# Performance work log

Hardware: AMD Instinct MI355X
Metric: run time of the kernel (lower is better)

## Reference

```python
import jax, jax.numpy as jnp
import numpy as np

N_NODES = 50000
N_USERS = 10000
N_STATE = 1024
N_T1 = 2048
N_T2 = 2048
N_EDGES = 4096


def setup_inputs() -> dict:
    key = jax.random.key(0)
    ks = jax.random.split(key, 10)
    d = N_STATE
    s_u = jax.random.normal(ks[0], (N_USERS, d), jnp.float32)
    x = jax.random.normal(ks[1], (N_NODES, d), jnp.float32)
    # Deterministic graph on which the original torch code is well-defined:
    # POI node 0 has one outgoing edge (edge 0) to tail node 1.
    # Tail node 1 receives edges from heads [0, 2, 3, ..., N_EDGES] in edge order,
    # so list-order in the torch loop aligns with edge-index order.
    heads = np.concatenate([[0], np.arange(2, N_EDGES + 1)]).astype(np.int64)
    tails = np.ones(N_EDGES, dtype=np.int64)
    edge_index = jnp.asarray(np.stack([heads, tails]))
    edge_attr = jax.random.normal(ks[2], (N_EDGES, d), jnp.float32)
    T = jax.random.normal(ks[3], (N_T1, N_T2), jnp.float32)
    u = lambda k, s: jax.random.uniform(k, s, jnp.float32, -1.0, 1.0)
    W_u = u(ks[4], (d, 1))
    W_p = u(ks[5], (d, 1))
    W_T_1 = u(ks[6], (d, N_T1))
    W_T_2 = u(ks[7], (N_T2, 1))
    b_T = u(ks[8], (d, 1))
    W_p_ = u(ks[9], (1, d))
    return dict(s_u=s_u, x=x, edge_attr=edge_attr, T=T, W_u=W_u, W_p=W_p,
                W_T_1=W_T_1, W_T_2=W_T_2, b_T=b_T, W_p_=W_p_,
                edge_index=edge_index, user_index=7, POI_index=0)


def reference(s_u, x, edge_attr, T, W_u, W_p, W_T_1, W_T_2, b_T, W_p_,
              edge_index, user_index, POI_index):
    N, d = x.shape
    heads, tails = edge_index[0], edge_index[1]
    # temporal context vector: sigmoid(W_T_1 @ T @ W_T_2 + b_T), shape (d,)
    t_vec = jax.nn.sigmoid(W_T_1 @ T @ W_T_2 + b_T)[:, 0]
    cur_user = s_u[user_index]   # (d,)
    cur_POI = x[POI_index]       # (d,)
    # user update: u' = sigmoid(u + W_u * (h_P . T'))
    s_u = s_u.at[user_index].set(
        jax.nn.sigmoid(cur_user + W_u[:, 0] * jnp.dot(cur_POI, t_vec)))
    # visited POI update: h' = sigmoid(h + W_p * (u . T'))
    new_POI = jax.nn.sigmoid(cur_POI + W_p[:, 0] * jnp.dot(cur_user, t_vec))
    x = x.at[POI_index].set(new_POI)
    # tail entities of the visited POI: x[tail] = new_POI + edge_attr[e]
    rel_mask = heads == POI_index
    dummy = jnp.zeros((1, d), x.dtype)
    tgt = jnp.where(rel_mask, tails, N)  # route masked-out edges to dummy row
    x = jnp.concatenate([x, dummy], 0).at[tgt].set(new_POI[None, :] + edge_attr)[:N]
    # neighboring POIs: edges whose tail is in the tail set; replicate the original
    # neigh_rel[POI_index] = False / neigh_index.remove(POI_index) pair, which by
    # construction both drop the edge at position POI_index.
    is_tail = jnp.zeros((N + 1,), bool).at[tgt].set(True)[:N]
    neigh_mask = is_tail[tails].at[POI_index].set(False)  # (E,)
    h_emb = x[heads]                        # (E, d), tail-updated embeddings
    scal = (h_emb - edge_attr) @ W_p_[0]    # (E,)  W_p_ . (x[head] - r)
    vals = jax.nn.sigmoid(h_emb + scal[:, None])
    tgt2 = jnp.where(neigh_mask, heads, N)
    x = jnp.concatenate([x, dummy], 0).at[tgt2].set(vals)[:N]
    return (s_u, x)
```

## Files before the change

### kernel.cpp

```cpp
#include <hip/hip_runtime.h>
#include <math.h>
#include <limits.h>

#define D 1024

typedef float f32x4 __attribute__((ext_vector_type(4)));

__device__ __forceinline__ float sigmoidf_(float v) {
    return 1.0f / (1.0f + expf(-v));
}

__device__ __forceinline__ float block_reduce_sum256(float v) {
    #pragma unroll
    for (int off = 32; off; off >>= 1) v += __shfl_down(v, off, 64);
    __shared__ float sm[4];
    int lane = threadIdx.x & 63, w = threadIdx.x >> 6;
    if (lane == 0) sm[w] = v;
    __syncthreads();
    float s = sm[0] + sm[1] + sm[2] + sm[3];
    __syncthreads();
    return s;
}

__global__ void k_pre(const float* __restrict__ T,
                      const float* __restrict__ w,
                      float* __restrict__ tmp,
                      int* __restrict__ flags,
                      int n_flags, int t4 ) {
    const int tid = threadIdx.x;
    int gid = blockIdx.x * 256 + tid;
    int gsz = gridDim.x * 256;
    for (int i = gid; i < n_flags; i += gsz) flags[i] = -1;

    const int row = blockIdx.x;
    const float4* Tr = (const float4*)(T + (size_t)row * (size_t)(t4 * 4));
    const float4* wv = (const float4*)w;
    float acc = 0.f;
    for (int i = tid; i < t4; i += 256) {
        float4 a = Tr[i], c = wv[i];
        acc += a.x * c.x + a.y * c.y + a.z * c.z + a.w * c.w;
    }
    float s = block_reduce_sum256(acc);
    if (tid == 0) tmp[row] = s;
}

__global__ void k_tvec2(const float* __restrict__ W_T_1,
                        const float* __restrict__ tmp,
                        const float* __restrict__ b_T,
                        const float* __restrict__ x,
                        const float* __restrict__ s_u,
                        const int* __restrict__ user_ptr,
                        const int* __restrict__ POI_ptr,
                        const int* __restrict__ edge_index,
                        int* __restrict__ tail_edge,
                        int* __restrict__ neigh_edge,
                        float* __restrict__ pu_P,
                        float* __restrict__ pu_U,
                        int k4 , int E) {
    const int tid = threadIdx.x;
    if (blockIdx.x == gridDim.x - 1) {
        const int POI = POI_ptr[0];
        for (int e = tid; e < E; e += 256)
            if (edge_index[e] == POI)
                atomicMax(&tail_edge[edge_index[E + e]], e);
        __syncthreads();
        for (int e = tid; e < E; e += 256) {
            if (e == POI) continue;
            int te = atomicMax(&tail_edge[edge_index[E + e]], INT_MIN);
            if (te >= 0) atomicMax(&neigh_edge[edge_index[e]], e);
        }
        return;
    }
    const int row = blockIdx.x;
    const float4* Wr = (const float4*)(W_T_1 + (size_t)row * (size_t)(k4 * 4));
    const float4* tv = (const float4*)tmp;
    float acc = 0.f;
    for (int i = tid; i < k4; i += 256) {
        float4 a = Wr[i], c = tv[i];
        acc += a.x * c.x + a.y * c.y + a.z * c.z + a.w * c.w;
    }
    float s = block_reduce_sum256(acc);
    if (tid == 0) {
        float t = sigmoidf_(s + b_T[row]);
        pu_P[row] = x[(size_t)POI_ptr[0] * D + row] * t;
        pu_U[row] = s_u[(size_t)user_ptr[0] * D + row] * t;
    }
}

__global__ void k_mega8(const float* __restrict__ s_u,
                        const float* __restrict__ x,
                        const float* __restrict__ edge_attr,
                        const float* __restrict__ W_u,
                        const float* __restrict__ W_p,
                        const float* __restrict__ Wp_row,
                        const int* __restrict__ user_ptr,
                        const int* __restrict__ POI_ptr,
                        const int* __restrict__ tail_edge,
                        const int* __restrict__ neigh_edge,
                        const float* __restrict__ pu_P,
                        const float* __restrict__ pu_U,
                        float* __restrict__ out,
                        int N_users, int total_rows) {
    const int tid = threadIdx.x;
    const int base = blockIdx.x * 8;
    const int user = user_ptr[0], POI = POI_ptr[0];

    f32x4 v[8];
    #pragma unroll
    for (int k = 0; k < 8; k++) {
        int r = base + k;
        if (r >= total_rows) continue;
        const float* src = (r < N_users) ? s_u + (size_t)r * D
                                         : x + (size_t)(r - N_users) * D;
        v[k] = *((const f32x4*)src + tid);
    }

    int te[8], ne[8];
    bool sp[8];
    #pragma unroll
    for (int k = 0; k < 8; k++) {
        int r = base + k;
        te[k] = -1; ne[k] = -1; sp[k] = false;
        if (r >= total_rows) continue;
        if (r < N_users) {
            sp[k] = (r == user);
        } else {
            int j = r - N_users;
            te[k] = tail_edge[j];
            ne[k] = neigh_edge[j];
            sp[k] = (te[k] >= 0) || (ne[k] >= 0) || (j == POI);
        }
    }

    #pragma unroll
    for (int k = 0; k < 8; k++) {
        int r = base + k;
        if (r >= total_rows) continue;
        f32x4* dst = (f32x4*)(out + (size_t)r * D) + tid;
        if (!sp[k]) {
            __builtin_nontemporal_store(v[k], dst);
            continue;
        }
        if (r < N_users) {
            f32x4 pp = ((const f32x4*)pu_P)[tid];
            float dotP = block_reduce_sum256(pp.x + pp.y + pp.z + pp.w);
            f32x4 wu = ((const f32x4*)W_u)[tid];
            f32x4 o;
            o.x = sigmoidf_(v[k].x + wu.x * dotP);
            o.y = sigmoidf_(v[k].y + wu.y * dotP);
            o.z = sigmoidf_(v[k].z + wu.z * dotP);
            o.w = sigmoidf_(v[k].w + wu.w * dotP);
            __builtin_nontemporal_store(o, dst);
            continue;
        }
        const int j = r - N_users;
        f32x4 uu = ((const f32x4*)pu_U)[tid];
        float dotU = block_reduce_sum256(uu.x + uu.y + uu.z + uu.w);
        f32x4 xp = ((const f32x4*)(x + (size_t)POI * D))[tid];
        f32x4 wp = ((const f32x4*)W_p)[tid];
        f32x4 np;
        np.x = sigmoidf_(xp.x + wp.x * dotU);
        np.y = sigmoidf_(xp.y + wp.y * dotU);
        np.z = sigmoidf_(xp.z + wp.z * dotU);
        np.w = sigmoidf_(xp.w + wp.w * dotU);
        f32x4 hv;
        if (te[k] >= 0) {
            f32x4 b = ((const f32x4*)(edge_attr + (size_t)te[k] * D))[tid];
            hv = np + b;
        } else if (j == POI) {
            hv = np;
        } else {
            hv = v[k];
        }
        if (ne[k] < 0) {
            __builtin_nontemporal_store(hv, dst);
            continue;
        }
        f32x4 ev = ((const f32x4*)(edge_attr + (size_t)ne[k] * D))[tid];
        f32x4 w = ((const f32x4*)Wp_row)[tid];
        f32x4 dd = hv - ev;
        float acc = dd.x * w.x + dd.y * w.y + dd.z * w.z + dd.w * w.w;
        float scal = block_reduce_sum256(acc);
        f32x4 o;
        o.x = sigmoidf_(hv.x + scal);
        o.y = sigmoidf_(hv.y + scal);
        o.z = sigmoidf_(hv.z + scal);
        o.w = sigmoidf_(hv.w + scal);
        __builtin_nontemporal_store(o, dst);
    }
}

extern "C" void kernel_launch(void* const* d_in, const int* in_sizes, int n_in,
                              void* d_out, int out_size, void* d_ws, size_t ws_size,
                              hipStream_t stream) {
    const float* s_u       = (const float*)d_in[0];
    const float* x         = (const float*)d_in[1];
    const float* edge_attr = (const float*)d_in[2];
    const float* T         = (const float*)d_in[3];
    const float* W_u       = (const float*)d_in[4];
    const float* W_p       = (const float*)d_in[5];
    const float* W_T_1     = (const float*)d_in[6];
    const float* W_T_2     = (const float*)d_in[7];
    const float* b_T       = (const float*)d_in[8];
    const float* W_p_      = (const float*)d_in[9];
    const int*   edge_index = (const int*)d_in[10];
    const int*   user_ptr   = (const int*)d_in[11];
    const int*   POI_ptr    = (const int*)d_in[12];

    const int E       = in_sizes[10] / 2;
    const int N_users = in_sizes[0] / D;
    const int N       = in_sizes[1] / D;
    const int N_T2    = in_sizes[7];
    const int N_T1    = in_sizes[6] / D;

    float* ws_f       = (float*)d_ws;
    float* tmp        = ws_f;
    float* pu_P       = ws_f + N_T1;
    float* pu_U       = pu_P + D;
    int*   tail_edge  = (int*)(pu_U + D);
    int*   neigh_edge = tail_edge + N;

    k_pre<<<N_T1, 256, 0, stream>>>(T, W_T_2, tmp, tail_edge, 2 * N, N_T2 / 4);

    k_tvec2<<<D + 1, 256, 0, stream>>>(W_T_1, tmp, b_T, x, s_u, user_ptr,
                                       POI_ptr, edge_index, tail_edge,
                                       neigh_edge, pu_P, pu_U, N_T1 / 4, E);

    const int total_rows = N_users + N;
    k_mega8<<<(total_rows + 7) / 8, 256, 0, stream>>>(
        s_u, x, edge_attr, W_u, W_p, W_p_, user_ptr, POI_ptr,
        tail_edge, neigh_edge, pu_P, pu_U, (float*)d_out, N_users, total_rows);
}
```

Before: 126.5 us.

## Split fused row kernel into bulk streaming copy plus sparse edge-fix kernel

Replaces the per-row mega kernel, which loaded every row and checked per-row flags, with a grid-stride nontemporal copy of s_u and x into the output. A second kernel, launched with one block per edge plus one extra block, then overwrites only the user row, the POI row and the rows touched by edges. The intent is to make the dominant copy a simple bandwidth-bound stream without per-row flag reads or branches. The cost is an extra launch and rows being written twice, and correctness now depends on the fix kernel running after the copy and on the per-edge predicates choosing exactly one writer per row.

```diff
diff --git a/kernel.cpp b/kernel.cpp
--- a/kernel.cpp
+++ b/kernel.cpp
@@ -87,96 +87,98 @@
     }
 }
 
-__global__ void k_mega8(const float* __restrict__ s_u,
-                        const float* __restrict__ x,
-                        const float* __restrict__ edge_attr,
-                        const float* __restrict__ W_u,
-                        const float* __restrict__ W_p,
-                        const float* __restrict__ Wp_row,
-                        const int* __restrict__ user_ptr,
-                        const int* __restrict__ POI_ptr,
-                        const int* __restrict__ tail_edge,
-                        const int* __restrict__ neigh_edge,
-                        const float* __restrict__ pu_P,
-                        const float* __restrict__ pu_U,
-                        float* __restrict__ out,
-                        int N_users, int total_rows) {
+__global__ void k_copy(const f32x4* __restrict__ su,
+                       const f32x4* __restrict__ xx,
+                       f32x4* __restrict__ out,
+                       int n4_su, int n4_x) {
+    const int gid = blockIdx.x * 256 + threadIdx.x;
+    const int gsz = gridDim.x * 256;
+    for (int i = gid; i < n4_su; i += gsz)
+        __builtin_nontemporal_store(__builtin_nontemporal_load(su + i), out + i);
+    f32x4* out_x = out + n4_su;
+    for (int i = gid; i < n4_x; i += gsz)
+        __builtin_nontemporal_store(__builtin_nontemporal_load(xx + i), out_x + i);
+}
+
+__global__ void k_fix(const float* __restrict__ s_u,
+                      const float* __restrict__ x,
+                      const float* __restrict__ edge_attr,
+                      const float* __restrict__ W_u,
+                      const float* __restrict__ W_p,
+                      const float* __restrict__ Wp_row,
+                      const int* __restrict__ user_ptr,
+                      const int* __restrict__ POI_ptr,
+                      const int* __restrict__ edge_index,
+                      const int* __restrict__ tail_edge,
+                      const int* __restrict__ neigh_edge,
+                      const float* __restrict__ pu_P,
+                      const float* __restrict__ pu_U,
+                      float* __restrict__ out,
+                      int N_users, int E) {
+    const int e = blockIdx.x;
     const int tid = threadIdx.x;
-    const int base = blockIdx.x * 8;
-    const int user = user_ptr[0], POI = POI_ptr[0];
-
-    f32x4 v[8];
-    #pragma unroll
-    for (int k = 0; k < 8; k++) {
-        int r = base + k;
-        if (r >= total_rows) continue;
-        const float* src = (r < N_users) ? s_u + (size_t)r * D
-                                         : x + (size_t)(r - N_users) * D;
-        v[k] = *((const f32x4*)src + tid);
-    }
-
-    int te[8], ne[8];
-    bool sp[8];
-    #pragma unroll
-    for (int k = 0; k < 8; k++) {
-        int r = base + k;
-        te[k] = -1; ne[k] = -1; sp[k] = false;
-        if (r >= total_rows) continue;
-        if (r < N_users) {
-            sp[k] = (r == user);
-        } else {
-            int j = r - N_users;
-            te[k] = tail_edge[j];
-            ne[k] = neigh_edge[j];
-            sp[k] = (te[k] >= 0) || (ne[k] >= 0) || (j == POI);
+    const int POI = POI_ptr[0];
+    float* out_x = out + (size_t)N_users * D;
+
+    if (e == E) {
+        const int user = user_ptr[0];
+        f32x4 pp = ((const f32x4*)pu_P)[tid];
+        float dotP = block_reduce_sum256(pp.x + pp.y + pp.z + pp.w);
+        f32x4 uv = ((const f32x4*)(s_u + (size_t)user * D))[tid];
+        f32x4 wu = ((const f32x4*)W_u)[tid];
+        f32x4 o;
+        o.x = sigmoidf_(uv.x + wu.x * dotP);
+        o.y = sigmoidf_(uv.y + wu.y * dotP);
+        o.z = sigmoidf_(uv.z + wu.z * dotP);
+        o.w = sigmoidf_(uv.w + wu.w * dotP);
+        __builtin_nontemporal_store(o, (f32x4*)(out + (size_t)user * D) + tid);
+        if (tail_edge[POI] < 0 && neigh_edge[POI] < 0) {
+            f32x4 uu = ((const f32x4*)pu_U)[tid];
+            float dotU = block_reduce_sum256(uu.x + uu.y + uu.z + uu.w);
+            f32x4 xp = ((const f32x4*)(x + (size_t)POI * D))[tid];
+            f32x4 wp = ((const f32x4*)W_p)[tid];
+            f32x4 np;
+            np.x = sigmoidf_(xp.x + wp.x * dotU);
+            np.y = sigmoidf_(xp.y + wp.y * dotU);
+            np.z = sigmoidf_(xp.z + wp.z * dotU);
+            np.w = sigmoidf_(xp.w + wp.w * dotU);
+            __builtin_nontemporal_store(np, (f32x4*)(out_x + (size_t)POI * D) + tid);
         }
-    }
-
-    #pragma unroll
-    for (int k = 0; k < 8; k++) {
-        int r = base + k;
-        if (r >= total_rows) continue;
-        f32x4* dst = (f32x4*)(out + (size_t)r * D) + tid;
-        if (!sp[k]) {
-            __builtin_nontemporal_store(v[k], dst);
-            continue;
-        }
-        if (r < N_users) {
-            f32x4 pp = ((const f32x4*)pu_P)[tid];
-            float dotP = block_reduce_sum256(pp.x + pp.y + pp.z + pp.w);
-            f32x4 wu = ((const f32x4*)W_u)[tid];
-            f32x4 o;
-            o.x = sigmoidf_(v[k].x + wu.x * dotP);
-            o.y = sigmoidf_(v[k].y + wu.y * dotP);
-            o.z = sigmoidf_(v[k].z + wu.z * dotP);
-            o.w = sigmoidf_(v[k].w + wu.w * dotP);
-            __builtin_nontemporal_store(o, dst);
-            continue;
-        }
-        const int j = r - N_users;
-        f32x4 uu = ((const f32x4*)pu_U)[tid];
-        float dotU = block_reduce_sum256(uu.x + uu.y + uu.z + uu.w);
-        f32x4 xp = ((const f32x4*)(x + (size_t)POI * D))[tid];
-        f32x4 wp = ((const f32x4*)W_p)[tid];
-        f32x4 np;
-        np.x = sigmoidf_(xp.x + wp.x * dotU);
-        np.y = sigmoidf_(xp.y + wp.y * dotU);
-        np.z = sigmoidf_(xp.z + wp.z * dotU);
-        np.w = sigmoidf_(xp.w + wp.w * dotU);
+        return;
+    }
+
+    const int h = edge_index[e], t = edge_index[E + e];
+    const bool tail_w  = (h == POI) && (tail_edge[t] == e) && (neigh_edge[t] < 0);
+    const bool neigh_w = (e != POI) && (tail_edge[t] >= 0) && (neigh_edge[h] == e);
+    if (!tail_w && !neigh_w) return;
+
+    f32x4 uu = ((const f32x4*)pu_U)[tid];
+    float dotU = block_reduce_sum256(uu.x + uu.y + uu.z + uu.w);
+    f32x4 xp = ((const f32x4*)(x + (size_t)POI * D))[tid];
+    f32x4 wp = ((const f32x4*)W_p)[tid];
+    f32x4 np;
+    np.x = sigmoidf_(xp.x + wp.x * dotU);
+    np.y = sigmoidf_(xp.y + wp.y * dotU);
+    np.z = sigmoidf_(xp.z + wp.z * dotU);
+    np.w = sigmoidf_(xp.w + wp.w * dotU);
+
+    if (tail_w) {
+        f32x4 b = ((const f32x4*)(edge_attr + (size_t)e * D))[tid];
+        __builtin_nontemporal_store(np + b, (f32x4*)(out_x + (size_t)t * D) + tid);
+    }
+
+    if (neigh_w) {
         f32x4 hv;
-        if (te[k] >= 0) {
-            f32x4 b = ((const f32x4*)(edge_attr + (size_t)te[k] * D))[tid];
+        const int be = tail_edge[h];
+        if (be >= 0) {
+            f32x4 b = ((const f32x4*)(edge_attr + (size_t)be * D))[tid];
             hv = np + b;
-        } else if (j == POI) {
+        } else if (h == POI) {
             hv = np;
         } else {
-            hv = v[k];
+            hv = ((const f32x4*)(x + (size_t)h * D))[tid];
         }
-        if (ne[k] < 0) {
-            __builtin_nontemporal_store(hv, dst);
-            continue;
-        }
-        f32x4 ev = ((const f32x4*)(edge_attr + (size_t)ne[k] * D))[tid];
+        f32x4 ev = ((const f32x4*)(edge_attr + (size_t)e * D))[tid];
         f32x4 w = ((const f32x4*)Wp_row)[tid];
         f32x4 dd = hv - ev;
         float acc = dd.x * w.x + dd.y * w.y + dd.z * w.z + dd.w * w.w;
@@ -186,7 +188,7 @@
         o.y = sigmoidf_(hv.y + scal);
         o.z = sigmoidf_(hv.z + scal);
         o.w = sigmoidf_(hv.w + scal);
-        __builtin_nontemporal_store(o, dst);
+        __builtin_nontemporal_store(o, (f32x4*)(out_x + (size_t)h * D) + tid);
     }
 }
 
@@ -226,8 +228,13 @@
                                        POI_ptr, edge_index, tail_edge,
                                        neigh_edge, pu_P, pu_U, N_T1 / 4, E);
 
-    const int total_rows = N_users + N;
-    k_mega8<<<(total_rows + 7) / 8, 256, 0, stream>>>(
-        s_u, x, edge_attr, W_u, W_p, W_p_, user_ptr, POI_ptr,
-        tail_edge, neigh_edge, pu_P, pu_U, (float*)d_out, N_users, total_rows);
-}
+    const int n4_su = (int)((size_t)N_users * D / 4);
+    const int n4_x  = (int)((size_t)N * D / 4);
+    k_copy<<<4096, 256, 0, stream>>>((const f32x4*)s_u, (const f32x4*)x,
+                                     (f32x4*)d_out, n4_su, n4_x);
+
+    k_fix<<<E + 1, 256, 0, stream>>>(s_u, x, edge_attr, W_u, W_p, W_p_,
+                                     user_ptr, POI_ptr, edge_index,
+                                     tail_edge, neigh_edge, pu_P, pu_U,
+                                     (float*)d_out, N_users, E);
+}
```

Measured after the change: 122.6 us. -3.1%, faster.
